# Performance work log

Measured on AMD Instinct MI355X. Metric: run time of the kernel, lower is better.

Reference implementation:

```python
import jax, jax.numpy as jnp
import numpy as np

NEG_INF = jnp.float32(-1e30)
HASH_PRIME = jnp.int32(1000003)
BLANK_INDEX = 0
BEAM_WIDTH = 32
TOP_PATHS = 1


def _beam_search_single(logp, length):
    """CTC prefix beam search for one utterance.
    logp: [T, C] log-probabilities. length: scalar int32.
    Returns (neg_log_prob [P], lengths [P], labels [P, T]).
    """
    T, C = logp.shape
    W = BEAM_WIDTH
    classes = jnp.arange(C, dtype=jnp.int32)
    tpos = jnp.arange(T, dtype=jnp.int32)
    N = W + W * C  # stay candidates + extend candidates

    seqs0 = jnp.zeros((W, T), jnp.int32)
    lens0 = jnp.zeros((W,), jnp.int32)
    hashes0 = jnp.arange(W, dtype=jnp.int32)  # distinct -> no spurious merging
    pb0 = jnp.full((W,), NEG_INF, jnp.float32).at[0].set(0.0)  # empty prefix, ends-in-blank
    pnb0 = jnp.full((W,), NEG_INF, jnp.float32)

    def step(state, inp):
        seqs, lens, hashes, pb, pnb = state
        lp, t = inp  # lp: [C]
        last = jnp.where(lens > 0, seqs[jnp.arange(W), jnp.maximum(lens - 1, 0)], -1)
        lp_last = jnp.where(last >= 0, lp[jnp.maximum(last, 0)], NEG_INF)
        ptot = jnp.logaddexp(pb, pnb)
        # --- stay candidates (same prefix): blank emission + repeated last label
        stay_pb = ptot + lp[BLANK_INDEX]
        stay_pnb = pnb + lp_last
        # --- extend candidates (W, C): prefix + c, c != blank
        ext_pnb = jnp.where(classes[None, :] == last[:, None],
                            pb[:, None] + lp[None, :],      # repeat label needs blank gap
                            ptot[:, None] + lp[None, :])
        ext_pnb = jnp.where(classes[None, :] == BLANK_INDEX, NEG_INF, ext_pnb)
        ext_pb = jnp.full((W, C), NEG_INF, jnp.float32)
        ext_hash = hashes[:, None] * HASH_PRIME + (classes[None, :] + 1)
        cand_pb = jnp.concatenate([stay_pb, ext_pb.reshape(-1)])
        cand_pnb = jnp.concatenate([stay_pnb, ext_pnb.reshape(-1)])
        cand_hash = jnp.concatenate([hashes, ext_hash.reshape(-1)])
        # --- merge candidates sharing the same prefix (by rolling hash)
        order = jnp.argsort(cand_hash)
        h_s = cand_hash[order]
        pb_s, pnb_s = cand_pb[order], cand_pnb[order]
        new_seg = jnp.concatenate([jnp.ones((1,), jnp.int32),
                                   (h_s[1:] != h_s[:-1]).astype(jnp.int32)])
        seg_id = jnp.cumsum(new_seg) - 1

        def seg_lse(x):
            m = jax.ops.segment_max(x, seg_id, num_segments=N)
            s = jax.ops.segment_sum(jnp.exp(x - m[seg_id]), seg_id, num_segments=N)
            return m + jnp.log(s)

        pb_m = seg_lse(pb_s)[seg_id]
        pnb_m = seg_lse(pnb_s)[seg_id]
        first = new_seg == 1
        pb_s = jnp.where(first, pb_m, NEG_INF)
        pnb_s = jnp.where(first, pnb_m, NEG_INF)
        tot = jnp.logaddexp(pb_s, pnb_s)
        # --- beam pruning
        _, top_idx = jax.lax.top_k(tot, W)
        sel = order[top_idx]  # indices into flat candidate list
        is_ext = sel >= W
        parent = jnp.where(is_ext, (sel - W) // C, sel)
        cls = jnp.where(is_ext, (sel - W) % C, 0).astype(jnp.int32)
        new_pb = pb_s[top_idx]
        new_pnb = pnb_s[top_idx]
        new_hash = cand_hash[sel]
        p_seqs = seqs[parent]
        p_lens = lens[parent]
        new_seqs = jnp.where(is_ext[:, None] & (tpos[None, :] == p_lens[:, None]),
                             cls[:, None], p_seqs)
        new_lens = p_lens + is_ext.astype(jnp.int32)
        # only advance while t < data_length
        active = t < length
        seqs = jnp.where(active, new_seqs, seqs)
        lens = jnp.where(active, new_lens, lens)
        hashes = jnp.where(active, new_hash, hashes)
        pb = jnp.where(active, new_pb, pb)
        pnb = jnp.where(active, new_pnb, pnb)
        return (seqs, lens, hashes, pb, pnb), None

    (seqs, lens, hashes, pb, pnb), _ = jax.lax.scan(
        step, (seqs0, lens0, hashes0, pb0, pnb0), (logp, tpos))
    tot = jnp.logaddexp(pb, pnb)
    top_tot, top_i = jax.lax.top_k(tot, TOP_PATHS)
    return -top_tot, lens[top_i], seqs[top_i]


def setup_inputs() -> dict:
    key = jax.random.key(0)
    k1, k2 = jax.random.split(key)
    data = jax.random.normal(k1, (512, 64, 128), jnp.float32)
    data = jax.nn.log_softmax(data, axis=-1)  # layer expects log probs (from_logits=False)
    data_length = jax.random.randint(k2, (64,), 1, 513, dtype=jnp.int32)
    return {"data": data, "data_length": data_length}


def reference(data, data_length):
    # data: [max_time, batch, num_classes] log probs -> [batch, T, C]
    logp = jnp.transpose(data, (1, 0, 2))
    probs, lengths, predicted = jax.vmap(_beam_search_single)(logp, data_length)
    # top_paths == 1 path of _select_most_likely_path: plain reshape
    B = predicted.shape[0]
    T = predicted.shape[2]
    best = predicted.reshape(B, T)
    lens = lengths.reshape(B)
    # _mask_out_junk_values: fill positions >= length with blank_index
    mask = jnp.arange(T, dtype=lens.dtype)[None, :] < lens[:, None]
    return jnp.where(mask, best, jnp.int32(BLANK_INDEX))
```

## Files before the change

### kernel.cpp

```cpp
#include <hip/hip_runtime.h>
#include <stdint.h>

#define T_MAX 512
#define BATCH 64
#define NCLS  128
#define BEAM  32
#define TBL   6144
#define NEGF  (-1e30f)
#define EMPTYK ((int)0x80000000)
#define HPRIME 1000003u
#define SCAP  256

__device__ __forceinline__ float lae(float a, float b) {
  float mx = fmaxf(a, b);
  return mx + log1pf(expf(-fabsf(a - b)));
}
__device__ __forceinline__ unsigned encf(float x) {
  unsigned b = __float_as_uint(x);
  return (b & 0x80000000u) ? ~b : (b | 0x80000000u);
}
__device__ __forceinline__ float decf(unsigned u) {
  unsigned b = (u & 0x80000000u) ? (u ^ 0x80000000u) : ~u;
  return __uint_as_float(b);
}

__device__ __forceinline__ int tbl_insert(int* key, int h) {
  unsigned x = (unsigned)h * 2654435761u;
  x ^= x >> 16;
  int j = (int)(((unsigned long long)x * (unsigned long long)TBL) >> 32);
  for (;;) {
    int cur = key[j];
    if (cur == EMPTYK) cur = atomicCAS(&key[j], EMPTYK, h);
    if (cur == EMPTYK || cur == h) return j;
    ++j; if (j == TBL) j = 0;
  }
}

__device__ __forceinline__ unsigned long long shflx64(unsigned long long v, int m) {
  unsigned lo = (unsigned)__shfl_xor((int)(unsigned)v, m, 64);
  unsigned hi = (unsigned)__shfl_xor((int)(unsigned)(v >> 32), m, 64);
  return ((unsigned long long)hi << 32) | lo;
}

__global__ __launch_bounds__(512, 1)
void ctc_beam_kernel(const float* __restrict__ data,
                     const int* __restrict__ dlen,
                     int* __restrict__ out) {
  __shared__ int       tkey[TBL];
  __shared__ unsigned  tmax[TBL];
  __shared__ unsigned  tsum[TBL];
  __shared__ unsigned  tmin[TBL];
  __shared__ unsigned short bp[T_MAX * BEAM];
  __shared__ float lpbuf[2][NCLS];
  __shared__ int   bhash[2][BEAM];
  __shared__ float bpb[2][BEAM], bpnb[2][BEAM];
  __shared__ int   blen[2][BEAM], blast[2][BEAM];
  __shared__ float sptot[BEAM], s_pb[BEAM], s_pnb[BEAM], s_pnbm[BEAM];
  __shared__ int   stay_slot[BEAM];
  __shared__ unsigned char mergeTo[BEAM * NCLS];
  __shared__ int mergeCnt[BEAM], mergeFrom[BEAM];
  __shared__ unsigned thsub[64];
  __shared__ int anom, ovf;
  __shared__ int scnt[2];
  __shared__ unsigned thr_s;
  __shared__ unsigned long long skey[SCAP];
  __shared__ unsigned sidx[SCAP];
  __shared__ unsigned long long wkey[8 * BEAM];
  __shared__ unsigned widx[8 * BEAM];
  __shared__ unsigned sel[BEAM];
  __shared__ int seqbuf[T_MAX];
  __shared__ int flen_s;

  const int tid = threadIdx.x;
  const int b = blockIdx.x;
  int L = dlen[b];
  L = L < 0 ? 0 : (L > T_MAX ? T_MAX : L);

  if (tid < BEAM) {
    bhash[0][tid] = tid;
    bpb[0][tid]   = (tid == 0) ? 0.0f : NEGF;
    bpnb[0][tid]  = NEGF;
    blen[0][tid]  = 0;
    blast[0][tid] = -1;
    mergeCnt[tid] = 0;
  }
  {
    unsigned* mtw = (unsigned*)mergeTo;
    for (int m = tid; m < (BEAM * NCLS) / 4; m += 512) mtw[m] = 0xFFFFFFFFu;
  }
  if (tid == 0) { anom = 1; ovf = 0; scnt[0] = 0; scnt[1] = 0; }
  if (tid < NCLS && L > 0) lpbuf[0][tid] = data[(size_t)b * NCLS + tid];
  __syncthreads();

  int cb = 0;
  for (int t = 0; t < L; ++t) {
    const int par = t & 1;
    const bool haspre = (tid >= 256) && (tid < 256 + NCLS) && (t + 1 < L);
    float pre = 0.0f;
    if (haspre) pre = data[((size_t)(t + 1) * BATCH + b) * NCLS + (tid - 256)];
    float* lpc = lpbuf[par];

    if (tid < BEAM) {
      const float pbv = bpb[cb][tid], pnbv = bpnb[cb][tid];
      const float pt = lae(pbv, pnbv);
      sptot[tid] = pt;
      s_pb[tid]  = pt + lpc[0];
      const int lsti = blast[cb][tid];
      s_pnb[tid] = pnbv + ((lsti >= 0) ? lpc[lsti] : NEGF);
      thsub[32 + tid] = 0u;
    }
    for (int k = tid; k < BEAM * BEAM; k += 512) {
      const int j = k >> 5, i2 = k & 31;
      const unsigned hj = (unsigned)bhash[cb][j];
      const unsigned hip = (unsigned)bhash[cb][i2] * HPRIME;
      const unsigned c = hj - hip - 1u;
      if (c < (unsigned)NCLS) {
        atomicAdd(&mergeCnt[j], 1);
        mergeFrom[j] = (i2 << 8) | (int)c;
        mergeTo[i2 * NCLS + (int)c] = (unsigned char)j;
      }
      if (j < i2) {
        const unsigned d = ((unsigned)bhash[cb][j] - (unsigned)bhash[cb][i2]) * HPRIME;
        if (d + 127u <= 254u) anom = 1;
      }
    }
    __syncthreads();

    const int i  = tid >> 4;
    const int c0 = (tid & 15) << 3;
    unsigned long long k8[8];
    {
      const float pbi = bpb[cb][i];
      const float pti = sptot[i];
      const int   lsti = blast[cb][i];
      const unsigned hb = (unsigned)bhash[cb][i] * HPRIME;
      const float4 l0 = ((const float4*)(lpc + c0))[0];
      const float4 l1 = ((const float4*)(lpc + c0))[1];
      const float lv[8] = {l0.x, l0.y, l0.z, l0.w, l1.x, l1.y, l1.z, l1.w};
      const unsigned m0 = ((const unsigned*)&mergeTo[i * NCLS + c0])[0];
      const unsigned m1 = ((const unsigned*)&mergeTo[i * NCLS + c0])[1];
      unsigned pbest = 0u;
      #pragma unroll
      for (int k = 0; k < 8; ++k) {
        const int c = c0 + k;
        const unsigned mb = ((k < 4 ? (m0 >> (8 * k)) : (m1 >> (8 * (k - 4)))) & 0xFFu);
        const float x = (c == 0) ? NEGF : (((c == lsti) ? pbi : pti) + lv[k]);
        const float tot = fmaxf(x, NEGF);
        const unsigned h = hb + (unsigned)(c + 1);
        unsigned long long key =
            ((unsigned long long)encf(tot) << 32) |
            (unsigned long long)(0xFFFFFFFFu - (h ^ 0x80000000u));
        if (mb != 0xFFu || c == 0) key = 0ull;
        k8[k] = key;
        const unsigned e32 = (unsigned)(key >> 32);
        pbest = pbest > e32 ? pbest : e32;
      }
      atomicMax(&thsub[32 + i], pbest);
    }
    if (tid < BEAM) {
      const int j = tid;
      if (mergeCnt[j] > 1) anom = 1;
      float pnbm;
      if (mergeCnt[j] == 1) {
        const int mf = mergeFrom[j];
        const int mi = mf >> 8, mc = mf & 255;
        const float e = (mc == 0) ? NEGF
            : (((mc == blast[cb][mi]) ? bpb[cb][mi] : sptot[mi]) + lpc[mc]);
        const float a = s_pnb[j];
        const float m = fmaxf(a, e);
        const float s = expf(a - m) + expf(e - m);
        pnbm = m + logf(s);
      } else {
        pnbm = s_pnb[j];
      }
      s_pnbm[j] = pnbm;
      thsub[j] = encf(lae(s_pb[j], pnbm));
    }
    if (tid == 511) scnt[par ^ 1] = 0;
    __syncthreads();

    const bool an = (anom != 0);
    bool dorare = an;
    if (!an) {
      if (tid < 64) {
        const unsigned vq = thsub[tid];
        int rank = 0;
        #pragma unroll 8
        for (int p = 0; p < 64; ++p) {
          const unsigned vp = thsub[p];
          rank += (vp > vq || (vp == vq && p < tid)) ? 1 : 0;
        }
        if (rank == 31) thr_s = vq;
      } else {
        unsigned* mtw = (unsigned*)mergeTo;
        for (int m = tid - 64; m < (BEAM * NCLS) / 4; m += 448) mtw[m] = 0xFFFFFFFFu;
        if (tid >= 64 && tid < 64 + BEAM) mergeCnt[tid - 64] = 0;
        if (haspre) lpbuf[par ^ 1][tid - 256] = pre;
      }
      __syncthreads();

      const unsigned thr = thr_s;
      int myn = 0;
      #pragma unroll
      for (int k = 0; k < 8; ++k) myn += ((unsigned)(k8[k] >> 32) >= thr) ? 1 : 0;
      const bool stayS = (tid < BEAM) && (thsub[tid] >= thr);
      myn += stayS ? 1 : 0;
      if (myn) {
        int o = atomicAdd(&scnt[par], myn);
        if (o + myn <= SCAP) {
          #pragma unroll
          for (int k = 0; k < 8; ++k) {
            if ((unsigned)(k8[k] >> 32) >= thr) {
              skey[o] = k8[k];
              sidx[o] = (unsigned)(BEAM + i * NCLS + (c0 + k));
              ++o;
            }
          }
          if (stayS) {
            skey[o] = ((unsigned long long)thsub[tid] << 32) |
                      (unsigned long long)(0xFFFFFFFFu - ((unsigned)bhash[cb][tid] ^ 0x80000000u));
            sidx[o] = (unsigned)tid;
          }
        } else ovf = 1;
      }
      __syncthreads();
      dorare = (ovf != 0);
    }

    if (!dorare) {
      const int scr = scnt[par];
      if (tid < scr) {
        const unsigned long long kq = skey[tid];
        int rank = 0;
        #pragma unroll 4
        for (int p = 0; p < scr; ++p) rank += (skey[p] > kq) ? 1 : 0;
        if (rank < BEAM) {
          const int j = rank;
          const unsigned s = sidx[tid];
          int nh, p, cls, ex; float npb, npnb;
          if (s < BEAM) {
            p = (int)s; cls = 0; ex = 0;
            nh = bhash[cb][p];
            npb = s_pb[p];
            npnb = s_pnbm[p];
          } else {
            const unsigned q = s - BEAM;
            p = (int)(q >> 7); cls = (int)(q & 127); ex = 1;
            nh = (int)((unsigned)bhash[cb][p] * HPRIME + (unsigned)(cls + 1));
            npb = NEGF;
            npnb = (cls == 0) ? NEGF
                 : (((cls == blast[cb][p]) ? bpb[cb][p] : sptot[p]) + lpc[cls]);
          }
          const int plen = blen[cb][p], plast = blast[cb][p];
          const int nb = cb ^ 1;
          bhash[nb][j] = nh; bpb[nb][j] = npb; bpnb[nb][j] = npnb;
          blen[nb][j]  = plen + ex;
          blast[nb][j] = ex ? cls : plast;
          bp[t * BEAM + j] = (unsigned short)(p | (cls << 5) | (ex << 12));
        }
      }
      __syncthreads();
    } else {
      for (int m = tid; m < TBL; m += 512) {
        tkey[m] = EMPTYK; tmax[m] = 0u; tsum[m] = 0u; tmin[m] = 0xFFFFFFFFu;
      }
      __syncthreads();

      int eslot[8]; float ex_[8];
      {
        const float pbi = bpb[cb][i];
        const float pti = sptot[i];
        const int   lsti = blast[cb][i];
        const unsigned hb = (unsigned)bhash[cb][i] * HPRIME;
        #pragma unroll
        for (int k = 0; k < 8; ++k) {
          const int c = c0 + k;
          int h = (int)(hb + (unsigned)(c + 1));
          if (h == EMPTYK) h = (int)0x80000001u;
          const float x = (c == 0) ? NEGF : (((c == lsti) ? pbi : pti) + lpc[c]);
          const int s = tbl_insert(tkey, h);
          atomicMax(&tmax[s], encf(x));
          atomicMin(&tmin[s], (unsigned)(BEAM + i * NCLS + c));
          eslot[k] = s; ex_[k] = x;
        }
      }
      if (tid < BEAM) {
        const int s = tbl_insert(tkey, bhash[cb][tid]);
        atomicMax(&tmax[s], encf(s_pnb[tid]));
        atomicMin(&tmin[s], (unsigned)tid);
        stay_slot[tid] = s;
      }
      __syncthreads();

      #pragma unroll
      for (int k = 0; k < 8; ++k) {
        const int s = eslot[k];
        atomicAdd((float*)&tsum[s], expf(ex_[k] - decf(tmax[s])));
      }
      if (tid < BEAM) {
        const int s = stay_slot[tid];
        atomicAdd((float*)&tsum[s], expf(s_pnb[tid] - decf(tmax[s])));
      }
      __syncthreads();

      for (int m = tid; m < TBL; m += 512) {
        if (tkey[m] != EMPTYK) {
          const float mm = decf(tmax[m]);
          const float ss = __uint_as_float(tsum[m]);
          const float pnbm = mm + logf(ss);
          tmax[m] = __float_as_uint(pnbm);
          tsum[m] = encf(lae(NEGF, pnbm));
        }
      }
      __syncthreads();
      if (tid < BEAM) {
        const int s = stay_slot[tid];
        tsum[s] = encf(lae(s_pb[tid], __uint_as_float(tmax[s])));
      }
      __syncthreads();

      {
        const int wv = tid >> 6, ln = tid & 63;
        const int base = wv * (TBL / 8) + ln * (TBL / 512);
        unsigned long long kk2[TBL / 512];
        #pragma unroll
        for (int m = 0; m < TBL / 512; ++m) {
          const int idx = base + m;
          if (tkey[idx] != EMPTYK) {
            const unsigned hh = (unsigned)tkey[idx] ^ 0x80000000u;
            kk2[m] = ((unsigned long long)tsum[idx] << 32) |
                     (unsigned long long)(0xFFFFFFFFu - hh);
          } else kk2[m] = 0ull;
        }
        unsigned cons = 0;
        for (int it = 0; it < BEAM; ++it) {
          unsigned long long best = 0ull; int bi = -1;
          #pragma unroll
          for (int m = 0; m < TBL / 512; ++m)
            if (!((cons >> m) & 1u) && kk2[m] > best) { best = kk2[m]; bi = m; }
          unsigned long long wm = best;
          #pragma unroll
          for (int off = 32; off > 0; off >>= 1) {
            const unsigned long long o = shflx64(wm, off);
            if (o > wm) wm = o;
          }
          const unsigned long long ball = __ballot(best == wm && wm != 0ull);
          const int winner = ball ? (__ffsll((long long)ball) - 1) : -1;
          if (ln == winner) {
            cons |= 1u << bi;
            wkey[wv * BEAM + it] = wm;
            widx[wv * BEAM + it] = (unsigned)(base + bi);
          } else if (winner < 0 && ln == 0) {
            wkey[wv * BEAM + it] = 0ull;
            widx[wv * BEAM + it] = 0xFFFFFFFFu;
          }
        }
      }
      __syncthreads();
      if (tid < 64) {
        unsigned long long kk2[4]; unsigned ii[4];
        #pragma unroll
        for (int m = 0; m < 4; ++m) { kk2[m] = wkey[tid * 4 + m]; ii[m] = widx[tid * 4 + m]; }
        unsigned cons = 0;
        for (int it = 0; it < BEAM; ++it) {
          unsigned long long best = 0ull; int bi = -1;
          #pragma unroll
          for (int m = 0; m < 4; ++m)
            if (!((cons >> m) & 1u) && kk2[m] > best) { best = kk2[m]; bi = m; }
          unsigned long long wm = best;
          #pragma unroll
          for (int off = 32; off > 0; off >>= 1) {
            const unsigned long long o = shflx64(wm, off);
            if (o > wm) wm = o;
          }
          const unsigned long long ball = __ballot(best == wm && wm != 0ull);
          const int winner = ball ? (__ffsll((long long)ball) - 1) : -1;
          if (tid == winner) { cons |= 1u << bi; sel[it] = ii[bi]; }
          else if (winner < 0 && tid == 0) sel[it] = 0xFFFFFFFFu;
        }
      }
      __syncthreads();

      if (tid < BEAM) {
        const int j = tid;
        const unsigned s = sel[j];
        int nh, p, cls, ex; float npb, npnb;
        if (s != 0xFFFFFFFFu) {
          nh = tkey[s];
          npnb = __uint_as_float(tmax[s]);
          npb = NEGF;
          #pragma unroll
          for (int q = 0; q < BEAM; ++q)
            if (stay_slot[q] == (int)s) npb = s_pb[q];
          const unsigned mi = tmin[s];
          ex  = (mi >= BEAM) ? 1 : 0;
          p   = ex ? (int)((mi - BEAM) >> 7) : (int)mi;
          cls = ex ? (int)((mi - BEAM) & 127) : 0;
          p &= 31;
        } else {
          nh = 0x7F000000 + j; npb = NEGF; npnb = NEGF; p = j; cls = 0; ex = 0;
        }
        const int plen = blen[cb][p], plast = blast[cb][p];
        const int nb = cb ^ 1;
        bhash[nb][j] = nh; bpb[nb][j] = npb; bpnb[nb][j] = npnb;
        blen[nb][j]  = plen + ex;
        blast[nb][j] = ex ? cls : plast;
        bp[t * BEAM + j] = (unsigned short)(p | (cls << 5) | (ex << 12));
      }
      {
        unsigned* mtw = (unsigned*)mergeTo;
        for (int m = tid; m < (BEAM * NCLS) / 4; m += 512) mtw[m] = 0xFFFFFFFFu;
      }
      if (tid >= 64 && tid < 64 + BEAM) mergeCnt[tid - 64] = 0;
      if (tid == 511) { anom = 0; ovf = 0; }
      if (haspre) lpbuf[par ^ 1][tid - 256] = pre;
      __syncthreads();
    }
    cb ^= 1;
  }

  if (tid == 0) {
    float bt = -3.4e38f; int bj = 0;
    for (int j = 0; j < BEAM; ++j) {
      const float tt = lae(bpb[cb][j], bpnb[cb][j]);
      if (tt > bt) { bt = tt; bj = j; }
    }
    int cur = bj;
    int pos = blen[cb][bj];
    flen_s = pos;
    for (int tt = L - 1; tt >= 0; --tt) {
      const unsigned short e = bp[tt * BEAM + cur];
      const int p = e & 31, cl = (e >> 5) & 127, ex = (e >> 12) & 1;
      if (ex) { --pos; if (pos >= 0) seqbuf[pos] = cl; }
      cur = p;
    }
  }
  __syncthreads();
  const int fl = flen_s;
  for (int k = tid; k < T_MAX; k += 512) {
    out[(size_t)b * T_MAX + k] = (k < fl) ? seqbuf[k] : 0;
  }
}

extern "C" void kernel_launch(void* const* d_in, const int* in_sizes, int n_in,
                              void* d_out, int out_size, void* d_ws, size_t ws_size,
                              hipStream_t stream) {
  const float* data = (const float*)d_in[0];
  const int*   dlen = (const int*)d_in[1];
  int* out = (int*)d_out;
  (void)in_sizes; (void)n_in; (void)out_size; (void)d_ws; (void)ws_size;
  hipLaunchKernelGGL(ctc_beam_kernel, dim3(BATCH), dim3(512), 0, stream,
                     data, dlen, out);
}
```

Baseline: 2.563 ms.

## Replace shared merge tables with register scans and wave-level prefix compaction

Removes the shared mergeTo/mergeCnt tables and the first per-step barrier. Each thread now recomputes merge masks by scanning the 32 beam hashes in registers, and the stay-candidate merge counts are computed by a dedicated warp range. Candidate compaction uses a wave-level prefix sum with one atomic per wavefront instead of per-thread atomics, and the rank loop is unrolled in chunks of 16 with padding. The goal is to cut barriers, table clears and atomic contention on the per-timestep serial path, at the cost of redundant hash comparisons per thread.

```diff
diff --git a/kernel.cpp b/kernel.cpp
--- a/kernel.cpp
+++ b/kernel.cpp
@@ -57,13 +57,11 @@
   __shared__ int   blen[2][BEAM], blast[2][BEAM];
   __shared__ float sptot[BEAM], s_pb[BEAM], s_pnb[BEAM], s_pnbm[BEAM];
   __shared__ int   stay_slot[BEAM];
-  __shared__ unsigned char mergeTo[BEAM * NCLS];
-  __shared__ int mergeCnt[BEAM], mergeFrom[BEAM];
   __shared__ unsigned thsub[64];
   __shared__ int anom, ovf;
   __shared__ int scnt[2];
   __shared__ unsigned thr_s;
-  __shared__ unsigned long long skey[SCAP];
+  __shared__ unsigned long long skey[SCAP + 16];
   __shared__ unsigned sidx[SCAP];
   __shared__ unsigned long long wkey[8 * BEAM];
   __shared__ unsigned widx[8 * BEAM];
@@ -82,13 +80,8 @@
     bpnb[0][tid]  = NEGF;
     blen[0][tid]  = 0;
     blast[0][tid] = -1;
-    mergeCnt[tid] = 0;
   }
-  {
-    unsigned* mtw = (unsigned*)mergeTo;
-    for (int m = tid; m < (BEAM * NCLS) / 4; m += 512) mtw[m] = 0xFFFFFFFFu;
-  }
-  if (tid == 0) { anom = 1; ovf = 0; scnt[0] = 0; scnt[1] = 0; }
+  if (tid == 0) { anom = 0; ovf = 0; scnt[0] = 0; scnt[1] = 0; }
   if (tid < NCLS && L > 0) lpbuf[0][tid] = data[(size_t)b * NCLS + tid];
   __syncthreads();
 
@@ -100,83 +93,90 @@
     if (haspre) pre = data[((size_t)(t + 1) * BATCH + b) * NCLS + (tid - 256)];
     float* lpc = lpbuf[par];
 
-    if (tid < BEAM) {
-      const float pbv = bpb[cb][tid], pnbv = bpnb[cb][tid];
-      const float pt = lae(pbv, pnbv);
-      sptot[tid] = pt;
-      s_pb[tid]  = pt + lpc[0];
-      const int lsti = blast[cb][tid];
-      s_pnb[tid] = pnbv + ((lsti >= 0) ? lpc[lsti] : NEGF);
-      thsub[32 + tid] = 0u;
-    }
-    for (int k = tid; k < BEAM * BEAM; k += 512) {
-      const int j = k >> 5, i2 = k & 31;
-      const unsigned hj = (unsigned)bhash[cb][j];
-      const unsigned hip = (unsigned)bhash[cb][i2] * HPRIME;
-      const unsigned c = hj - hip - 1u;
-      if (c < (unsigned)NCLS) {
-        atomicAdd(&mergeCnt[j], 1);
-        mergeFrom[j] = (i2 << 8) | (int)c;
-        mergeTo[i2 * NCLS + (int)c] = (unsigned char)j;
-      }
-      if (j < i2) {
-        const unsigned d = ((unsigned)bhash[cb][j] - (unsigned)bhash[cb][i2]) * HPRIME;
-        if (d + 127u <= 254u) anom = 1;
-      }
-    }
-    __syncthreads();
-
     const int i  = tid >> 4;
     const int c0 = (tid & 15) << 3;
     unsigned long long k8[8];
     {
-      const float pbi = bpb[cb][i];
-      const float pti = sptot[i];
+      const float pbi = bpb[cb][i], pnbi = bpnb[cb][i];
+      const float pti = lae(pbi, pnbi);
       const int   lsti = blast[cb][i];
       const unsigned hb = (unsigned)bhash[cb][i] * HPRIME;
+      unsigned mmask = 0;
+      #pragma unroll
+      for (int j = 0; j < BEAM; ++j) {
+        const unsigned c = (unsigned)bhash[cb][j] - hb - 1u;
+        if ((c - (unsigned)c0) < 8u) mmask |= 1u << (c - (unsigned)c0);
+      }
       const float4 l0 = ((const float4*)(lpc + c0))[0];
       const float4 l1 = ((const float4*)(lpc + c0))[1];
       const float lv[8] = {l0.x, l0.y, l0.z, l0.w, l1.x, l1.y, l1.z, l1.w};
-      const unsigned m0 = ((const unsigned*)&mergeTo[i * NCLS + c0])[0];
-      const unsigned m1 = ((const unsigned*)&mergeTo[i * NCLS + c0])[1];
       unsigned pbest = 0u;
       #pragma unroll
       for (int k = 0; k < 8; ++k) {
         const int c = c0 + k;
-        const unsigned mb = ((k < 4 ? (m0 >> (8 * k)) : (m1 >> (8 * (k - 4)))) & 0xFFu);
         const float x = (c == 0) ? NEGF : (((c == lsti) ? pbi : pti) + lv[k]);
         const float tot = fmaxf(x, NEGF);
         const unsigned h = hb + (unsigned)(c + 1);
         unsigned long long key =
             ((unsigned long long)encf(tot) << 32) |
             (unsigned long long)(0xFFFFFFFFu - (h ^ 0x80000000u));
-        if (mb != 0xFFu || c == 0) key = 0ull;
+        if (((mmask >> k) & 1u) || c == 0) key = 0ull;
         k8[k] = key;
         const unsigned e32 = (unsigned)(key >> 32);
         pbest = pbest > e32 ? pbest : e32;
       }
-      atomicMax(&thsub[32 + i], pbest);
-    }
-    if (tid < BEAM) {
-      const int j = tid;
-      if (mergeCnt[j] > 1) anom = 1;
+      #pragma unroll
+      for (int m = 1; m <= 8; m <<= 1) {
+        const unsigned o = (unsigned)__shfl_xor((int)pbest, m, 64);
+        pbest = pbest > o ? pbest : o;
+      }
+      if ((tid & 15) == 0) thsub[32 + i] = pbest;
+    }
+    for (int k = tid; k < BEAM * BEAM; k += 512) {
+      const int j = k >> 5, i2 = k & 31;
+      if (j < i2) {
+        const unsigned d = ((unsigned)bhash[cb][j] - (unsigned)bhash[cb][i2]) * HPRIME;
+        if (d + 127u <= 254u) anom = 1;
+      }
+    }
+    unsigned skreg = 0, hjreg = 0;
+    if (tid >= 448 && tid < 448 + BEAM) {
+      const int j = tid - 448;
+      const float pbv = bpb[cb][j], pnbv = bpnb[cb][j];
+      const float pt = lae(pbv, pnbv);
+      sptot[j] = pt;
+      const float spb = pt + lpc[0];
+      s_pb[j] = spb;
+      const int lstj = blast[cb][j];
+      const float spnb = pnbv + ((lstj >= 0) ? lpc[lstj] : NEGF);
+      s_pnb[j] = spnb;
+      const unsigned hj = (unsigned)bhash[cb][j];
+      hjreg = hj;
+      int cnt = 0, from = 0;
+      #pragma unroll
+      for (int i2 = 0; i2 < BEAM; ++i2) {
+        const unsigned c = hj - (unsigned)bhash[cb][i2] * HPRIME - 1u;
+        if (c < (unsigned)NCLS) { ++cnt; from = (i2 << 8) | (int)c; }
+      }
+      if (cnt > 1) anom = 1;
       float pnbm;
-      if (mergeCnt[j] == 1) {
-        const int mf = mergeFrom[j];
-        const int mi = mf >> 8, mc = mf & 255;
+      if (cnt == 1) {
+        const int mi = from >> 8, mc = from & 255;
+        const float pti2 = lae(bpb[cb][mi], bpnb[cb][mi]);
         const float e = (mc == 0) ? NEGF
-            : (((mc == blast[cb][mi]) ? bpb[cb][mi] : sptot[mi]) + lpc[mc]);
-        const float a = s_pnb[j];
+            : (((mc == blast[cb][mi]) ? bpb[cb][mi] : pti2) + lpc[mc]);
+        const float a = spnb;
         const float m = fmaxf(a, e);
         const float s = expf(a - m) + expf(e - m);
         pnbm = m + logf(s);
       } else {
-        pnbm = s_pnb[j];
+        pnbm = spnb;
       }
       s_pnbm[j] = pnbm;
-      thsub[j] = encf(lae(s_pb[j], pnbm));
-    }
-    if (tid == 511) scnt[par ^ 1] = 0;
+      skreg = encf(lae(spb, pnbm));
+      thsub[j] = skreg;
+    }
+    if (tid == 447) scnt[par ^ 1] = 0;
     __syncthreads();
 
     const bool an = (anom != 0);
@@ -185,43 +185,49 @@
       if (tid < 64) {
         const unsigned vq = thsub[tid];
         int rank = 0;
-        #pragma unroll 8
+        #pragma unroll
         for (int p = 0; p < 64; ++p) {
           const unsigned vp = thsub[p];
           rank += (vp > vq || (vp == vq && p < tid)) ? 1 : 0;
         }
         if (rank == 31) thr_s = vq;
-      } else {
-        unsigned* mtw = (unsigned*)mergeTo;
-        for (int m = tid - 64; m < (BEAM * NCLS) / 4; m += 448) mtw[m] = 0xFFFFFFFFu;
-        if (tid >= 64 && tid < 64 + BEAM) mergeCnt[tid - 64] = 0;
-        if (haspre) lpbuf[par ^ 1][tid - 256] = pre;
-      }
+      }
+      if (haspre) lpbuf[par ^ 1][tid - 256] = pre;
       __syncthreads();
 
       const unsigned thr = thr_s;
-      int myn = 0;
+      const int ln = tid & 63;
+      const bool stayS = (tid >= 448) && (tid < 448 + BEAM) && (skreg >= thr);
+      int myn = stayS ? 1 : 0;
       #pragma unroll
       for (int k = 0; k < 8; ++k) myn += ((unsigned)(k8[k] >> 32) >= thr) ? 1 : 0;
-      const bool stayS = (tid < BEAM) && (thsub[tid] >= thr);
-      myn += stayS ? 1 : 0;
-      if (myn) {
-        int o = atomicAdd(&scnt[par], myn);
-        if (o + myn <= SCAP) {
-          #pragma unroll
-          for (int k = 0; k < 8; ++k) {
-            if ((unsigned)(k8[k] >> 32) >= thr) {
-              skey[o] = k8[k];
-              sidx[o] = (unsigned)(BEAM + i * NCLS + (c0 + k));
-              ++o;
-            }
-          }
-          if (stayS) {
-            skey[o] = ((unsigned long long)thsub[tid] << 32) |
-                      (unsigned long long)(0xFFFFFFFFu - ((unsigned)bhash[cb][tid] ^ 0x80000000u));
-            sidx[o] = (unsigned)tid;
-          }
-        } else ovf = 1;
+      int pfx = myn;
+      #pragma unroll
+      for (int d = 1; d < 64; d <<= 1) {
+        const int o = __shfl_up(pfx, d, 64);
+        if (ln >= d) pfx += o;
+      }
+      const int wtot = __shfl(pfx, 63, 64);
+      int wbase = 0;
+      if (ln == 0 && wtot) wbase = atomicAdd(&scnt[par], wtot);
+      wbase = __shfl(wbase, 0, 64);
+      if (wbase + wtot > SCAP) {
+        if (ln == 0 && wtot) ovf = 1;
+      } else if (myn) {
+        int o = wbase + pfx - myn;
+        #pragma unroll
+        for (int k = 0; k < 8; ++k) {
+          if ((unsigned)(k8[k] >> 32) >= thr) {
+            skey[o] = k8[k];
+            sidx[o] = (unsigned)(BEAM + i * NCLS + (c0 + k));
+            ++o;
+          }
+        }
+        if (stayS) {
+          skey[o] = ((unsigned long long)skreg << 32) |
+                    (unsigned long long)(0xFFFFFFFFu - (hjreg ^ 0x80000000u));
+          sidx[o] = (unsigned)(tid - 448);
+        }
       }
       __syncthreads();
       dorare = (ovf != 0);
@@ -232,8 +238,13 @@
       if (tid < scr) {
         const unsigned long long kq = skey[tid];
         int rank = 0;
-        #pragma unroll 4
-        for (int p = 0; p < scr; ++p) rank += (skey[p] > kq) ? 1 : 0;
+        for (int p0 = 0; p0 < scr; p0 += 16) {
+          #pragma unroll
+          for (int pp = 0; pp < 16; ++pp) {
+            const unsigned long long kp = skey[p0 + pp];
+            rank += ((p0 + pp) < scr && kp > kq) ? 1 : 0;
+          }
+        }
         if (rank < BEAM) {
           const int j = rank;
           const unsigned s = sidx[tid];
@@ -407,11 +418,6 @@
         blast[nb][j] = ex ? cls : plast;
         bp[t * BEAM + j] = (unsigned short)(p | (cls << 5) | (ex << 12));
       }
-      {
-        unsigned* mtw = (unsigned*)mergeTo;
-        for (int m = tid; m < (BEAM * NCLS) / 4; m += 512) mtw[m] = 0xFFFFFFFFu;
-      }
-      if (tid >= 64 && tid < 64 + BEAM) mergeCnt[tid - 64] = 0;
       if (tid == 511) { anom = 0; ovf = 0; }
       if (haspre) lpbuf[par ^ 1][tid - 256] = pre;
       __syncthreads();
```

New measurement: 3.404 ms. 1.33x slower.
